# Performance work log

Measured on AMD Instinct MI355X. Metric: run time of the kernel, lower is better.

The kernel has to match this reference:

```python
import jax, jax.numpy as jnp
import numpy as np


def setup_inputs() -> dict:
    key = jax.random.key(0)
    k1, _ = jax.random.split(key)
    N, H, CH, T = 4, 8, 64, 2048
    qkv = jax.random.normal(k1, (N, H * 3 * CH, T), dtype=jnp.float32)
    rescale = jnp.ones((1,), dtype=jnp.float32)
    return {"qkv": qkv, "rescale": rescale, "n_heads": H}


def reference(qkv, rescale, n_heads):
    bs, width, length = qkv.shape
    ch = width // (3 * n_heads)
    # [N, H*3*C, T] -> [N*H, 3*C, T] -> three [N*H, C, T]
    qkv_h = qkv.reshape(bs * n_heads, 3 * ch, length)
    q, k, v = qkv_h[:, :ch], qkv_h[:, ch:2 * ch], qkv_h[:, 2 * ch:]
    scale = 1.0 / jnp.sqrt(jnp.sqrt(jnp.float32(ch)))
    # scores: [B*H, T, S]
    weight = jnp.einsum('bct,bcs->bts', q * scale, k * scale)
    weight = jax.nn.softmax(weight.astype(jnp.float32) * rescale[0], axis=-1).astype(qkv.dtype)
    a = jnp.einsum('bts,bcs->bct', weight, v)  # [B*H, C, T]
    return a.reshape(bs, n_heads * ch, length)
```

## Files before the change

kernel.cpp:

```cpp
#include <hip/hip_runtime.h>
#include <stdint.h>

typedef _Float16 half8 __attribute__((ext_vector_type(8)));
typedef _Float16 half4 __attribute__((ext_vector_type(4)));
typedef __fp16   fp16x2 __attribute__((ext_vector_type(2)));
typedef float    floatx4 __attribute__((ext_vector_type(4)));

#define T_LEN 2048
#define CH 64
#define BH 32
#define QTILE 128
#define LDP 72
#define PTP 72
#define FRAG_BH 131072

__global__ __launch_bounds__(256, 2)
void prep_kernel(const float* __restrict__ qkv, const float* __restrict__ rescale,
                 _Float16* __restrict__ ws)
{
    __shared__ _Float16 Qs[64][LDP];
    __shared__ _Float16 Ks[64][LDP];
    __shared__ _Float16 Vs[64][LDP];

    const int tid  = threadIdx.x;
    const int bh   = blockIdx.y;
    const int tile = blockIdx.x;
    const int x0   = tile * 64;

    const float qscale = 0.125f * 1.4426950408889634f * rescale[0];

    const float* qp = qkv + (size_t)(bh >> 3) * (1536 * T_LEN)
                          + (size_t)(bh & 7) * (192 * T_LEN);
    const float* kp = qp + 64 * T_LEN;
    const float* vp = qp + 128 * T_LEN;

    {
        const int a4 = (tid & 15) * 4;
        const int c4 = (tid >> 4) * 4;
        float4 rq[4], rk[4];
#pragma unroll
        for (int i = 0; i < 4; ++i) {
            rq[i] = *(const float4*)(qp + (size_t)(c4 + i) * T_LEN + x0 + a4);
            rk[i] = *(const float4*)(kp + (size_t)(c4 + i) * T_LEN + x0 + a4);
        }
#pragma unroll
        for (int j = 0; j < 4; ++j) {
            half4 hq, hk;
#pragma unroll
            for (int i = 0; i < 4; ++i) {
                hq[i] = (_Float16)((&rq[i].x)[j] * qscale);
                hk[i] = (_Float16)((&rk[i].x)[j]);
            }
            *(half4*)&Qs[a4 + j][c4] = hq;
            *(half4*)&Ks[a4 + j][c4] = hk;
        }
        const int s4 = (tid & 15) * 4;
        const int cv = tid >> 4;
#pragma unroll
        for (int i = 0; i < 4; ++i) {
            const int c = cv + 16 * i;
            float4 r = *(const float4*)(vp + (size_t)c * T_LEN + x0 + s4);
            half4 h; h[0]=(_Float16)r.x; h[1]=(_Float16)r.y; h[2]=(_Float16)r.z; h[3]=(_Float16)r.w;
            *(half4*)&Vs[c][s4] = h;
        }
    }
    __syncthreads();

    const int lane = tid & 63, wave = tid >> 6;
    const int l15 = lane & 15, quad = lane >> 4;
    _Float16* qf = ws;
    _Float16* kf = ws + (size_t)BH * FRAG_BH;
    _Float16* vf = ws + (size_t)2 * BH * FRAG_BH;

#pragma unroll
    for (int ks = 0; ks < 2; ++ks) {
        half8 hq = *(const half8*)&Qs[wave * 16 + l15][ks * 32 + quad * 8];
        half8 hk = *(const half8*)&Ks[wave * 16 + l15][ks * 32 + quad * 8];
        half8 hv = *(const half8*)&Vs[wave * 16 + l15][ks * 32 + quad * 8];
        const size_t gqk = (((size_t)bh * 128 + tile * 4 + wave) * 2 + ks) * 512 + lane * 8;
        *(half8*)(qf + gqk) = hq;
        *(half8*)(kf + gqk) = hk;
        *(half8*)(vf + (((size_t)bh * 32 + tile) * 8 + wave * 2 + ks) * 512 + lane * 8) = hv;
    }
}

__device__ __forceinline__ void gload16(const _Float16* g, _Float16* l) {
    __builtin_amdgcn_global_load_lds(
        (const __attribute__((address_space(1))) void*)g,
        (__attribute__((address_space(3))) void*)l, 16, 0, 0);
}

__global__ __launch_bounds__(256, 2)
void attn_kernel(const _Float16* __restrict__ ws, float* __restrict__ out)
{
    __shared__ _Float16 Kb[2][4096];
    __shared__ _Float16 Vb[2][4096];
    __shared__ _Float16 Pt[4][32][PTP];

    const int tid  = threadIdx.x;
    const int wave = tid >> 6;
    const int lane = tid & 63;
    const int l15  = lane & 15;
    const int quad = lane >> 4;

    const int bid  = blockIdx.x;
    const int xcd  = bid & 7;
    const int slot = bid >> 3;
    const int bh   = (slot >> 4) * 8 + xcd;
    const int tile = slot & 15;
    const int t0   = tile * QTILE;

    const _Float16* qf = ws;
    const _Float16* kf = ws + (size_t)BH * FRAG_BH;
    const _Float16* vf = ws + (size_t)2 * BH * FRAG_BH;
    float* op = out + (size_t)bh * (CH * T_LEN);

    const _Float16* ktile = kf + (size_t)bh * FRAG_BH;
    const _Float16* vtile = vf + (size_t)bh * FRAG_BH;

    auto stage = [&](int st, int buf) {
        const _Float16* kg = ktile + (size_t)st * 4096 + wave * 1024 + lane * 8;
        const _Float16* vg = vtile + (size_t)st * 4096 + wave * 1024 + lane * 8;
        _Float16* kl = &Kb[buf][wave * 1024];
        _Float16* vl = &Vb[buf][wave * 1024];
        gload16(kg,       kl);
        gload16(kg + 512, kl + 512);
        gload16(vg,       vl);
        gload16(vg + 512, vl + 512);
    };

    half8 bq[2][2];
#pragma unroll
    for (int tb = 0; tb < 2; ++tb)
#pragma unroll
        for (int ks = 0; ks < 2; ++ks)
            bq[tb][ks] = *(const half8*)(qf +
                (((size_t)bh * 128 + tile * 8 + wave * 2 + tb) * 2 + ks) * 512 + lane * 8);

    const floatx4 fzero = {0.f, 0.f, 0.f, 0.f};
    floatx4 oacc[2][4];
#pragma unroll
    for (int tb = 0; tb < 2; ++tb)
#pragma unroll
        for (int ct = 0; ct < 4; ++ct) oacc[tb][ct] = fzero;
    floatx4 lacc[2] = {fzero, fzero};

    half8 bones;
#pragma unroll
    for (int i = 0; i < 8; ++i) bones[i] = (_Float16)1.0f;

    half8 ak[4][2];
    half8 bv[4][2];
    half8 ap[2][2];

    auto read_ak = [&](int buf) {
#pragma unroll
        for (int mt = 0; mt < 4; ++mt)
#pragma unroll
            for (int ks = 0; ks < 2; ++ks)
                ak[mt][ks] = *(const half8*)&Kb[buf][(mt * 2 + ks) * 512 + lane * 8];
    };
    auto read_bv = [&](int buf) {
#pragma unroll
        for (int ct = 0; ct < 4; ++ct)
#pragma unroll
            for (int ks = 0; ks < 2; ++ks)
                bv[ct][ks] = *(const half8*)&Vb[buf][(ct * 2 + ks) * 512 + lane * 8];
    };

    auto do_qk_exp = [&]() {
        floatx4 sacc[4][2];
#pragma unroll
        for (int mt = 0; mt < 4; ++mt)
#pragma unroll
            for (int tb = 0; tb < 2; ++tb) sacc[mt][tb] = fzero;
#pragma unroll
        for (int mt = 0; mt < 4; ++mt)
#pragma unroll
            for (int tb = 0; tb < 2; ++tb)
#pragma unroll
                for (int ks = 0; ks < 2; ++ks)
                    sacc[mt][tb] = __builtin_amdgcn_mfma_f32_16x16x32_f16(
                        ak[mt][ks], bq[tb][ks], sacc[mt][tb], 0, 0, 0);

#pragma unroll
        for (int mt = 0; mt < 4; ++mt)
#pragma unroll
            for (int tb = 0; tb < 2; ++tb) {
                fp16x2 p01 = __builtin_amdgcn_cvt_pkrtz(
                    __builtin_amdgcn_exp2f(sacc[mt][tb][0]),
                    __builtin_amdgcn_exp2f(sacc[mt][tb][1]));
                fp16x2 p23 = __builtin_amdgcn_cvt_pkrtz(
                    __builtin_amdgcn_exp2f(sacc[mt][tb][2]),
                    __builtin_amdgcn_exp2f(sacc[mt][tb][3]));
                half4 ph;
                ph[0] = (_Float16)p01[0]; ph[1] = (_Float16)p01[1];
                ph[2] = (_Float16)p23[0]; ph[3] = (_Float16)p23[1];
                *(half4*)&Pt[wave][tb * 16 + l15][mt * 16 + quad * 4] = ph;
            }
#pragma unroll
        for (int tb = 0; tb < 2; ++tb)
#pragma unroll
            for (int ks = 0; ks < 2; ++ks)
                ap[tb][ks] = *(const half8*)&Pt[wave][tb * 16 + l15][ks * 32 + quad * 8];
    };

    stage(0, 0);
    __syncthreads();
    read_ak(0);
    read_bv(0);
    stage(1, 1);
    do_qk_exp();
    __syncthreads();
    read_ak(1);

    for (int st = 1; st < 32; ++st) {
        const int cur = st & 1;
        if (st < 31) stage(st + 1, cur ^ 1);

#pragma unroll
        for (int tb = 0; tb < 2; ++tb)
#pragma unroll
            for (int ks = 0; ks < 2; ++ks)
                lacc[tb] = __builtin_amdgcn_mfma_f32_16x16x32_f16(ap[tb][ks], bones, lacc[tb], 0, 0, 0);
#pragma unroll
        for (int tb = 0; tb < 2; ++tb)
#pragma unroll
            for (int ct = 0; ct < 4; ++ct)
#pragma unroll
                for (int ks = 0; ks < 2; ++ks)
                    oacc[tb][ct] = __builtin_amdgcn_mfma_f32_16x16x32_f16(
                        ap[tb][ks], bv[ct][ks], oacc[tb][ct], 0, 0, 0);

        do_qk_exp();

        read_bv(cur);

        __syncthreads();
        if (st < 31) read_ak(cur ^ 1);
    }

#pragma unroll
    for (int tb = 0; tb < 2; ++tb)
#pragma unroll
        for (int ks = 0; ks < 2; ++ks)
            lacc[tb] = __builtin_amdgcn_mfma_f32_16x16x32_f16(ap[tb][ks], bones, lacc[tb], 0, 0, 0);
#pragma unroll
    for (int tb = 0; tb < 2; ++tb)
#pragma unroll
        for (int ct = 0; ct < 4; ++ct)
#pragma unroll
            for (int ks = 0; ks < 2; ++ks)
                oacc[tb][ct] = __builtin_amdgcn_mfma_f32_16x16x32_f16(
                    ap[tb][ks], bv[ct][ks], oacc[tb][ct], 0, 0, 0);

#pragma unroll
    for (int tb = 0; tb < 2; ++tb) {
        float linv[4];
#pragma unroll
        for (int r = 0; r < 4; ++r) linv[r] = 1.0f / lacc[tb][r];
#pragma unroll
        for (int ct = 0; ct < 4; ++ct) {
            const int c = ct * 16 + l15;
            const int t = t0 + wave * 32 + tb * 16 + quad * 4;
            float4 o;
#pragma unroll
            for (int r = 0; r < 4; ++r)
                (&o.x)[r] = oacc[tb][ct][r] * linv[r];
            *(float4*)(op + (size_t)c * T_LEN + t) = o;
        }
    }
}

extern "C" void kernel_launch(void* const* d_in, const int* in_sizes, int n_in,
                              void* d_out, int out_size, void* d_ws, size_t ws_size,
                              hipStream_t stream) {
    const float* qkv     = (const float*)d_in[0];
    const float* rescale = (const float*)d_in[1];
    float* out = (float*)d_out;
    _Float16* ws = (_Float16*)d_ws;

    prep_kernel<<<dim3(32, BH), dim3(256), 0, stream>>>(qkv, rescale, ws);
    attn_kernel<<<dim3(T_LEN / QTILE * BH), dim3(256), 0, stream>>>(ws, out);
}
```

Before: 132.3 us.

## Keep softmax probabilities in registers and feed PV MFMA without LDS round-trip

```diff
diff --git a/kernel.cpp b/kernel.cpp
--- a/kernel.cpp
+++ b/kernel.cpp
@@ -5,13 +5,13 @@
 typedef _Float16 half4 __attribute__((ext_vector_type(4)));
 typedef __fp16   fp16x2 __attribute__((ext_vector_type(2)));
 typedef float    floatx4 __attribute__((ext_vector_type(4)));
+typedef unsigned uintx2 __attribute__((ext_vector_type(2)));
 
 #define T_LEN 2048
 #define CH 64
 #define BH 32
 #define QTILE 128
 #define LDP 72
-#define PTP 72
 #define FRAG_BH 131072
 
 __global__ __launch_bounds__(256, 2)
@@ -76,11 +76,15 @@
     for (int ks = 0; ks < 2; ++ks) {
         half8 hq = *(const half8*)&Qs[wave * 16 + l15][ks * 32 + quad * 8];
         half8 hk = *(const half8*)&Ks[wave * 16 + l15][ks * 32 + quad * 8];
-        half8 hv = *(const half8*)&Vs[wave * 16 + l15][ks * 32 + quad * 8];
         const size_t gqk = (((size_t)bh * 128 + tile * 4 + wave) * 2 + ks) * 512 + lane * 8;
         *(half8*)(qf + gqk) = hq;
         *(half8*)(kf + gqk) = hk;
-        *(half8*)(vf + (((size_t)bh * 32 + tile) * 8 + wave * 2 + ks) * 512 + lane * 8) = hv;
+    }
+#pragma unroll
+    for (int ct = 0; ct < 4; ++ct) {
+        half4 hv = *(const half4*)&Vs[ct * 16 + l15][wave * 16 + quad * 4];
+        *(half4*)(vf + (size_t)bh * FRAG_BH
+                     + ((size_t)(tile * 4 + wave) * 4 + ct) * 256 + lane * 4) = hv;
     }
 }
 
@@ -95,7 +99,6 @@
 {
     __shared__ _Float16 Kb[2][4096];
     __shared__ _Float16 Vb[2][4096];
-    __shared__ _Float16 Pt[4][32][PTP];
 
     const int tid  = threadIdx.x;
     const int wave = tid >> 6;
@@ -138,20 +141,15 @@
                 (((size_t)bh * 128 + tile * 8 + wave * 2 + tb) * 2 + ks) * 512 + lane * 8);
 
     const floatx4 fzero = {0.f, 0.f, 0.f, 0.f};
-    floatx4 oacc[2][4];
-#pragma unroll
-    for (int tb = 0; tb < 2; ++tb)
-#pragma unroll
-        for (int ct = 0; ct < 4; ++ct) oacc[tb][ct] = fzero;
-    floatx4 lacc[2] = {fzero, fzero};
-
-    half8 bones;
-#pragma unroll
-    for (int i = 0; i < 8; ++i) bones[i] = (_Float16)1.0f;
+    floatx4 oacc[4][2];
+#pragma unroll
+    for (int ct = 0; ct < 4; ++ct)
+#pragma unroll
+        for (int tb = 0; tb < 2; ++tb) oacc[ct][tb] = fzero;
+    float lsum[2] = {0.f, 0.f};
 
     half8 ak[4][2];
-    half8 bv[4][2];
-    half8 ap[2][2];
+    half4 bv[4][4];
 
     auto read_ak = [&](int buf) {
 #pragma unroll
@@ -162,47 +160,46 @@
     };
     auto read_bv = [&](int buf) {
 #pragma unroll
-        for (int ct = 0; ct < 4; ++ct)
-#pragma unroll
-            for (int ks = 0; ks < 2; ++ks)
-                bv[ct][ks] = *(const half8*)&Vb[buf][(ct * 2 + ks) * 512 + lane * 8];
-    };
-
-    auto do_qk_exp = [&]() {
-        floatx4 sacc[4][2];
-#pragma unroll
         for (int mt = 0; mt < 4; ++mt)
 #pragma unroll
-            for (int tb = 0; tb < 2; ++tb) sacc[mt][tb] = fzero;
-#pragma unroll
-        for (int mt = 0; mt < 4; ++mt)
-#pragma unroll
-            for (int tb = 0; tb < 2; ++tb)
-#pragma unroll
-                for (int ks = 0; ks < 2; ++ks)
-                    sacc[mt][tb] = __builtin_amdgcn_mfma_f32_16x16x32_f16(
-                        ak[mt][ks], bq[tb][ks], sacc[mt][tb], 0, 0, 0);
-
-#pragma unroll
-        for (int mt = 0; mt < 4; ++mt)
-#pragma unroll
-            for (int tb = 0; tb < 2; ++tb) {
-                fp16x2 p01 = __builtin_amdgcn_cvt_pkrtz(
-                    __builtin_amdgcn_exp2f(sacc[mt][tb][0]),
-                    __builtin_amdgcn_exp2f(sacc[mt][tb][1]));
-                fp16x2 p23 = __builtin_amdgcn_cvt_pkrtz(
-                    __builtin_amdgcn_exp2f(sacc[mt][tb][2]),
-                    __builtin_amdgcn_exp2f(sacc[mt][tb][3]));
-                half4 ph;
-                ph[0] = (_Float16)p01[0]; ph[1] = (_Float16)p01[1];
-                ph[2] = (_Float16)p23[0]; ph[3] = (_Float16)p23[1];
-                *(half4*)&Pt[wave][tb * 16 + l15][mt * 16 + quad * 4] = ph;
+            for (int ct = 0; ct < 4; ++ct)
+                bv[mt][ct] = *(const half4*)&Vb[buf][mt * 1024 + ct * 256 + lane * 4];
+    };
+
+    auto body = [&]() {
+#pragma unroll
+        for (int mt = 0; mt < 4; ++mt) {
+            floatx4 s0 = fzero, s1 = fzero;
+#pragma unroll
+            for (int ks = 0; ks < 2; ++ks) {
+                s0 = __builtin_amdgcn_mfma_f32_16x16x32_f16(ak[mt][ks], bq[0][ks], s0, 0, 0, 0);
+                s1 = __builtin_amdgcn_mfma_f32_16x16x32_f16(ak[mt][ks], bq[1][ks], s1, 0, 0, 0);
             }
-#pragma unroll
-        for (int tb = 0; tb < 2; ++tb)
-#pragma unroll
-            for (int ks = 0; ks < 2; ++ks)
-                ap[tb][ks] = *(const half8*)&Pt[wave][tb * 16 + l15][ks * 32 + quad * 8];
+            float a0 = __builtin_amdgcn_exp2f(s0[0]);
+            float a1 = __builtin_amdgcn_exp2f(s0[1]);
+            float a2 = __builtin_amdgcn_exp2f(s0[2]);
+            float a3 = __builtin_amdgcn_exp2f(s0[3]);
+            float b0 = __builtin_amdgcn_exp2f(s1[0]);
+            float b1 = __builtin_amdgcn_exp2f(s1[1]);
+            float b2 = __builtin_amdgcn_exp2f(s1[2]);
+            float b3 = __builtin_amdgcn_exp2f(s1[3]);
+            lsum[0] += (a0 + a1) + (a2 + a3);
+            lsum[1] += (b0 + b1) + (b2 + b3);
+            uintx2 u0, u1;
+            u0[0] = __builtin_bit_cast(unsigned, __builtin_amdgcn_cvt_pkrtz(a0, a1));
+            u0[1] = __builtin_bit_cast(unsigned, __builtin_amdgcn_cvt_pkrtz(a2, a3));
+            u1[0] = __builtin_bit_cast(unsigned, __builtin_amdgcn_cvt_pkrtz(b0, b1));
+            u1[1] = __builtin_bit_cast(unsigned, __builtin_amdgcn_cvt_pkrtz(b2, b3));
+            half4 p0 = __builtin_bit_cast(half4, u0);
+            half4 p1 = __builtin_bit_cast(half4, u1);
+#pragma unroll
+            for (int ct = 0; ct < 4; ++ct) {
+                oacc[ct][0] = __builtin_amdgcn_mfma_f32_16x16x16f16(
+                    bv[mt][ct], p0, oacc[ct][0], 0, 0, 0);
+                oacc[ct][1] = __builtin_amdgcn_mfma_f32_16x16x16f16(
+                    bv[mt][ct], p1, oacc[ct][1], 0, 0, 0);
+            }
+        }
     };
 
     stage(0, 0);
@@ -210,65 +207,34 @@
     read_ak(0);
     read_bv(0);
     stage(1, 1);
-    do_qk_exp();
-    __syncthreads();
-    read_ak(1);
-
-    for (int st = 1; st < 32; ++st) {
+
+    for (int st = 0; st < 32; ++st) {
         const int cur = st & 1;
-        if (st < 31) stage(st + 1, cur ^ 1);
-
-#pragma unroll
-        for (int tb = 0; tb < 2; ++tb)
-#pragma unroll
-            for (int ks = 0; ks < 2; ++ks)
-                lacc[tb] = __builtin_amdgcn_mfma_f32_16x16x32_f16(ap[tb][ks], bones, lacc[tb], 0, 0, 0);
-#pragma unroll
-        for (int tb = 0; tb < 2; ++tb)
-#pragma unroll
-            for (int ct = 0; ct < 4; ++ct)
-#pragma unroll
-                for (int ks = 0; ks < 2; ++ks)
-                    oacc[tb][ct] = __builtin_amdgcn_mfma_f32_16x16x32_f16(
-                        ap[tb][ks], bv[ct][ks], oacc[tb][ct], 0, 0, 0);
-
-        do_qk_exp();
-
-        read_bv(cur);
-
-        __syncthreads();
-        if (st < 31) read_ak(cur ^ 1);
-    }
-
-#pragma unroll
-    for (int tb = 0; tb < 2; ++tb)
-#pragma unroll
-        for (int ks = 0; ks < 2; ++ks)
-            lacc[tb] = __builtin_amdgcn_mfma_f32_16x16x32_f16(ap[tb][ks], bones, lacc[tb], 0, 0, 0);
-#pragma unroll
-    for (int tb = 0; tb < 2; ++tb)
+        if (st >= 1 && st < 31) stage(st + 1, cur ^ 1);
+        body();
+        if (st < 31) {
+            __syncthreads();
+            read_ak(cur ^ 1);
+            read_bv(cur ^ 1);
+        }
+    }
+
+    float linv[2];
+#pragma unroll
+    for (int tb = 0; tb < 2; ++tb) {
+        float v = lsum[tb];
+        v += __shfl_xor(v, 16, 64);
+        v += __shfl_xor(v, 32, 64);
+        linv[tb] = 1.0f / v;
+    }
+#pragma unroll
+    for (int tb = 0; tb < 2; ++tb) {
+        const int t = t0 + wave * 32 + tb * 16 + l15;
 #pragma unroll
         for (int ct = 0; ct < 4; ++ct)
 #pragma unroll
-            for (int ks = 0; ks < 2; ++ks)
-                oacc[tb][ct] = __builtin_amdgcn_mfma_f32_16x16x32_f16(
-                    ap[tb][ks], bv[ct][ks], oacc[tb][ct], 0, 0, 0);
-
-#pragma unroll
-    for (int tb = 0; tb < 2; ++tb) {
-        float linv[4];
-#pragma unroll
-        for (int r = 0; r < 4; ++r) linv[r] = 1.0f / lacc[tb][r];
-#pragma unroll
-        for (int ct = 0; ct < 4; ++ct) {
-            const int c = ct * 16 + l15;
-            const int t = t0 + wave * 32 + tb * 16 + quad * 4;
-            float4 o;
-#pragma unroll
             for (int r = 0; r < 4; ++r)
-                (&o.x)[r] = oacc[tb][ct][r] * linv[r];
-            *(float4*)(op + (size_t)c * T_LEN + t) = o;
-        }
+                op[(size_t)(ct * 16 + quad * 4 + r) * T_LEN + t] = oacc[ct][tb][r] * linv[tb];
     }
 }
 
```

New measurement: 133.1 us. Within noise of the previous version (+0.6%).
